# Performance work log

Hardware: AMD Instinct MI355X
Metric: run time of the kernel (lower is better)

## Reference

```python
import jax, jax.numpy as jnp
import numpy as np

EPS = 1e-5

def yat_dense(x, kernel, bias, alpha):
    # scaled by (sqrt(F)/log(1+F))**alpha, plus bias.
    y = x @ kernel  # [..., F]
    dist = jnp.sum(x * x, axis=-1, keepdims=True) + jnp.sum(kernel * kernel, axis=0) - 2.0 * y
    out = (y * y) / (dist + EPS)
    F = kernel.shape[1]
    scale = (jnp.sqrt(jnp.float32(F)) / jnp.log1p(jnp.float32(F))) ** alpha
    return out * scale + bias

def setup_inputs() -> dict:
    key = jax.random.key(0)
    ks = jax.random.split(key, 8)
    B, T, C = 8, 1024, 1024
    x = jax.random.normal(ks[0], (B, T, C), dtype=jnp.float32)
    mask = jnp.tril(jnp.ones((T, T), dtype=bool))[None, None, :, :]  # causal [1,1,T,T]
    W_attn = jax.random.normal(ks[1], (C, 3 * C), dtype=jnp.float32) * (C ** -0.5)
    b_attn = jnp.zeros((3 * C,), dtype=jnp.float32)
    alpha_attn = jnp.ones((1,), dtype=jnp.float32)
    W_proj = jax.random.normal(ks[2], (C, C), dtype=jnp.float32) * (C ** -0.5)
    b_proj = jnp.zeros((C,), dtype=jnp.float32)
    alpha_proj = jnp.ones((1,), dtype=jnp.float32)
    return {"x": x, "mask": mask, "W_attn": W_attn, "b_attn": b_attn,
            "alpha_attn": alpha_attn, "W_proj": W_proj, "b_proj": b_proj,
            "alpha_proj": alpha_proj}

def reference(x, mask, W_attn, b_attn, alpha_attn, W_proj, b_proj, alpha_proj):
    B, T, C = x.shape
    H = 16
    hd = C // H
    qkv = yat_dense(x, W_attn, b_attn, alpha_attn)           # [B,T,3C]
    qkv = qkv.reshape(B, T, 3 * H, hd)
    q, k, v = jnp.array_split(qkv, 3, axis=2)                # each [B,T,H,hd]
    scale = 1.0 / jnp.sqrt(jnp.float32(hd))
    attn = jnp.einsum('bqhd,bkhd->bhqk', q, k) * scale       # [B,H,T,T]
    attn = jnp.where(mask, attn, jnp.finfo(jnp.float32).min)
    attn = jax.nn.softmax(attn, axis=-1)
    out = jnp.einsum('bhqk,bkhd->bqhd', attn, v).reshape(B, T, C)
    out = yat_dense(out, W_proj, b_proj, alpha_proj)         # [B,T,C]
    return out
```

## Files before the change

### kernel.cpp

```cpp
#include <hip/hip_runtime.h>
#include <math.h>

#define EPS 1e-5f
#define QSCALE 0.18033688011f

typedef short s16x8 __attribute__((ext_vector_type(8)));
typedef float f32x4 __attribute__((ext_vector_type(4)));
typedef unsigned short ushort_t;
typedef unsigned int uint_t;

__device__ inline ushort_t f2bf(float f) {
  uint_t u = __float_as_uint(f);
  uint_t r = (u + 0x7fffu + ((u >> 16) & 1u)) >> 16;
  return (ushort_t)r;
}
__device__ inline float bf2f(ushort_t h) {
  return __uint_as_float(((uint_t)h) << 16);
}
__device__ inline uint_t cvtpk_bf16(float lo, float hi) {
  uint_t r;
  asm("v_cvt_pk_bf16_f32 %0, %1, %2" : "=v"(r) : "v"(lo), "v"(hi));
  return r;
}

__global__ __launch_bounds__(256) void cast_norm_k(const float* __restrict__ x,
                                                   ushort_t* __restrict__ xbf,
                                                   float* __restrict__ xnorm) {
  const int row = blockIdx.x * 4 + (threadIdx.x >> 6);
  const int lane = threadIdx.x & 63;
  const float4* p = (const float4*)(x + (size_t)row * 1024);
  ushort4* o = (ushort4*)(xbf + (size_t)row * 1024);
  float s = 0.f;
#pragma unroll
  for (int i = lane; i < 256; i += 64) {
    float4 v = p[i];
    s += v.x * v.x + v.y * v.y + v.z * v.z + v.w * v.w;
    o[i] = make_ushort4(f2bf(v.x), f2bf(v.y), f2bf(v.z), f2bf(v.w));
  }
#pragma unroll
  for (int off = 1; off < 64; off <<= 1) s += __shfl_xor(s, off, 64);
  if (lane == 0) xnorm[row] = s;
}

__global__ __launch_bounds__(256) void transpose_cast_k(
    const float* __restrict__ W, ushort_t* __restrict__ o, int K, int N) {
  __shared__ float t[32][33];
  const int n0 = blockIdx.x * 32, k0 = blockIdx.y * 32;
  const int tx = threadIdx.x & 31, ty = threadIdx.x >> 5;
#pragma unroll
  for (int j = 0; j < 4; ++j)
    t[ty + j * 8][tx] = W[(size_t)(k0 + ty + j * 8) * N + n0 + tx];
  __syncthreads();
#pragma unroll
  for (int j = 0; j < 4; ++j)
    o[(size_t)(n0 + ty + j * 8) * K + k0 + tx] = f2bf(t[tx][ty + j * 8]);
}

__global__ __launch_bounds__(256) void rownorm_bf16_k(const ushort_t* __restrict__ X,
                                                      float* __restrict__ out, int K) {
  const int row = blockIdx.x * 4 + (threadIdx.x >> 6);
  const int lane = threadIdx.x & 63;
  const ushort4* p = (const ushort4*)(X + (size_t)row * K);
  float s = 0.f;
  const int nq = K >> 2;
  for (int i = lane; i < nq; i += 64) {
    ushort4 v = p[i];
    float a = bf2f(v.x), b = bf2f(v.y), c = bf2f(v.z), d = bf2f(v.w);
    s += a * a + b * b + c * c + d * d;
  }
#pragma unroll
  for (int off = 1; off < 64; off <<= 1) s += __shfl_xor(s, off, 64);
  if (lane == 0) out[row] = s;
}

template <int MODE, int KK>
__global__ __launch_bounds__(256) void gemm_yat_mfma(
    const ushort_t* __restrict__ abf, const ushort_t* __restrict__ btbf,
    const float* __restrict__ bias, const float* __restrict__ alpha,
    const float* __restrict__ rown, const float* __restrict__ coln,
    void* __restrict__ outp, ushort_t* __restrict__ vtp, int M, int N) {
  __shared__ alignas(16) short lds[2 * 16384];

  const int tid = threadIdx.x;
  const int wid = tid >> 6;
  const int lane = tid & 63;
  const int g = lane >> 4;
  const int wm = wid >> 1, wn = wid & 1;

  const int nbx = gridDim.x;
  const int id = blockIdx.y * nbx + blockIdx.x;
  const int xcd = id & 7;
  const int sq = id >> 3;
  const int gq = sq >> 6;
  const int rr = sq & 63;
  const int bm = (xcd * 8 + (rr >> 3)) * 128;
  const int bn = (gq * 8 + (rr & 7)) * 128;

  f32x4 acc[4][4];
#pragma unroll
  for (int m = 0; m < 4; ++m)
#pragma unroll
    for (int n = 0; n < 4; ++n) acc[m][n] = (f32x4){0.f, 0.f, 0.f, 0.f};

  const int kc_sw = ((lane & 3) - ((lane >> 3) & 3)) & 3;
  const int slot_rd = (g + ((lane & 15) >> 1)) & 3;

  const ushort_t* srcb[8];
#pragma unroll
  for (int j = 0; j < 8; ++j) {
    const int q = wid + 4 * j;
    const int reg_idx = q >> 4;
    const int grp = (q >> 1) & 7;
    const int half = q & 1;
    const int grow = grp * 16 + (lane >> 2);
    const int gcol = half * 32 + kc_sw * 8;
    srcb[j] = (reg_idx == 0) ? abf + (size_t)(bm + grow) * KK + gcol
                             : btbf + (size_t)(bn + grow) * KK + gcol;
  }

  auto stage = [&](int buf, int t) {
#pragma unroll
    for (int j = 0; j < 8; ++j) {
      const int q = wid + 4 * j;
      const int reg_idx = q >> 4;
      const int grp = (q >> 1) & 7;
      const int half = q & 1;
      short* dst = &lds[buf * 16384 + reg_idx * 8192 + grp * 1024 + half * 512];
      __builtin_amdgcn_global_load_lds(
          (const __attribute__((address_space(1))) void*)(srcb[j] + t * 64),
          (__attribute__((address_space(3))) void*)dst, 16, 0, 0);
    }
  };

  stage(0, 0);
  stage(1, 1);

  constexpr int NT = KK / 64;
#pragma unroll
  for (int t = 0; t < NT; ++t) {
    const int cur = t & 1;
    if (t < NT - 1) {
      asm volatile("s_waitcnt vmcnt(8)" ::: "memory");
    } else {
      asm volatile("s_waitcnt vmcnt(0)" ::: "memory");
    }
    __builtin_amdgcn_sched_barrier(0);
    __builtin_amdgcn_s_barrier();

    s16x8 af[2][4], bfr[2][4];
#pragma unroll
    for (int kk = 0; kk < 2; ++kk) {
#pragma unroll
      for (int m = 0; m < 4; ++m) {
        const int off = cur * 16384 + (wm * 4 + m) * 1024 + kk * 512 +
                        (lane & 15) * 32 + slot_rd * 8;
        af[kk][m] = *(const s16x8*)&lds[off];
      }
#pragma unroll
      for (int n = 0; n < 4; ++n) {
        const int off = cur * 16384 + 8192 + (wn * 4 + n) * 1024 + kk * 512 +
                        (lane & 15) * 32 + slot_rd * 8;
        bfr[kk][n] = *(const s16x8*)&lds[off];
      }
    }
    __builtin_amdgcn_sched_barrier(0);
    asm volatile("s_waitcnt lgkmcnt(0)" ::: "memory");
    __builtin_amdgcn_sched_barrier(0);
    __builtin_amdgcn_s_barrier();

    if (t + 2 < NT) stage(cur, t + 2);

    __builtin_amdgcn_s_setprio(1);
#pragma unroll
    for (int kk = 0; kk < 2; ++kk)
#pragma unroll
      for (int m = 0; m < 4; ++m)
#pragma unroll
        for (int n = 0; n < 4; ++n)
          acc[m][n] = __builtin_amdgcn_mfma_f32_16x16x32_bf16(af[kk][m], bfr[kk][n],
                                                              acc[m][n], 0, 0, 0);
    __builtin_amdgcn_s_setprio(0);
  }

  const float sc = powf(sqrtf((float)N) / log1pf((float)N), alpha[0]);
  const int r0 = (lane >> 4) * 4;
  const int c0 = lane & 15;
#pragma unroll
  for (int m = 0; m < 4; ++m) {
    const int rowb = bm + wm * 64 + m * 16 + r0;
    float rn[4] = {rown[rowb], rown[rowb + 1], rown[rowb + 2], rown[rowb + 3]};
#pragma unroll
    for (int n = 0; n < 4; ++n) {
      const int col = bn + wn * 64 + n * 16 + c0;
      const float cn = coln[col];
      const float bs = bias[col];
      f32x4 a = acc[m][n];
      float o4[4];
#pragma unroll
      for (int r = 0; r < 4; ++r) {
        const float y = a[r];
        const float dist = rn[r] + cn - 2.f * y + EPS;
        o4[r] = (y * y) / dist * sc + bs;
      }
      if (MODE == 1) {
        if (col < 1024) {
#pragma unroll
          for (int r = 0; r < 4; ++r) o4[r] *= QSCALE;
        }
        if (col >= 2048) {
          const int d = col & 63, hh = (col >> 6) & 15;
          const int bb = rowb >> 10, t0 = rowb & 1023;
          ushort4 pk = make_ushort4(f2bf(o4[0]), f2bf(o4[1]), f2bf(o4[2]), f2bf(o4[3]));
          *(ushort4*)(vtp + (((size_t)(bb * 16 + hh) * 64 + d) << 10) + t0) = pk;
        } else {
#pragma unroll
          for (int r = 0; r < 4; ++r)
            ((ushort_t*)outp)[(size_t)(rowb + r) * N + col] = f2bf(o4[r]);
        }
      } else {
#pragma unroll
        for (int r = 0; r < 4; ++r)
          ((float*)outp)[(size_t)(rowb + r) * N + col] = o4[r];
      }
    }
  }
}

__global__ __launch_bounds__(256) void attn_mfma_k(const ushort_t* __restrict__ qkv,
                                                   const ushort_t* __restrict__ vt,
                                                   ushort_t* __restrict__ out) {
  const int i = blockIdx.y * 8 + blockIdx.x;
  const int xcd = i & 7, s = i >> 3;
  const int bh = xcd * 16 + (s & 15);
  const int pairx = s >> 4;
  const int b = bh >> 4, h = bh & 15;

  const int tid = threadIdx.x;
  const int wid = tid >> 6;
  const int lane = tid & 63;
  const int g = lane >> 4;
  const int c = lane & 15;

  __shared__ alignas(16) ushort_t Ks[64][76];
  __shared__ alignas(16) ushort_t Vs[64][76];
  __shared__ alignas(16) ushort_t Pl[4][16][76];

  const int srow = tid >> 3;
  const int sd0 = (tid & 7) * 8;
  const ushort_t* kbase = qkv + (size_t)(b * 1024) * 3072 + 1024 + h * 64;
  const ushort_t* vbase = vt + ((size_t)(b * 16 + h) << 16);

#pragma unroll
  for (int pass = 0; pass < 2; ++pass) {
    const int qt = pass == 0 ? pairx : 15 - pairx;

    const ushort_t* qrow =
        qkv + ((size_t)(b * 1024 + qt * 64 + wid * 16 + c)) * 3072 + h * 64;
    s16x8 qf[2];
    qf[0] = *(const s16x8*)(qrow + g * 8);
    qf[1] = *(const s16x8*)(qrow + 32 + g * 8);

    f32x4 acc_o[4];
#pragma unroll
    for (int dt = 0; dt < 4; ++dt) acc_o[dt] = (f32x4){0.f, 0.f, 0.f, 0.f};
    float l_lane = 0.f;

    s16x8 kreg[2], vreg[2];
#pragma unroll
    for (int ii = 0; ii < 2; ++ii) {
      kreg[ii] = *(const s16x8*)(kbase + (size_t)(srow + ii * 32) * 3072 + sd0);
      vreg[ii] = *(const s16x8*)(vbase + (size_t)(srow + ii * 32) * 1024 + sd0);
    }

    for (int kt = 0; kt <= qt; ++kt) {
      __syncthreads();
#pragma unroll
      for (int ii = 0; ii < 2; ++ii) {
        *(s16x8*)&Ks[srow + ii * 32][sd0] = kreg[ii];
        *(s16x8*)&Vs[srow + ii * 32][sd0] = vreg[ii];
      }
      __syncthreads();

      if (kt < qt) {
#pragma unroll
        for (int ii = 0; ii < 2; ++ii) {
          kreg[ii] = *(const s16x8*)(kbase +
                                     (size_t)((kt + 1) * 64 + srow + ii * 32) * 3072 + sd0);
          vreg[ii] = *(const s16x8*)(vbase + (size_t)(srow + ii * 32) * 1024 +
                                     (kt + 1) * 64 + sd0);
        }
      }

      const bool diag = (kt == qt);
      const int jtmax = diag ? wid : 3;

      f32x4 sacc[4];
#pragma unroll
      for (int jt = 0; jt < 4; ++jt) sacc[jt] = (f32x4){0.f, 0.f, 0.f, 0.f};
      __builtin_amdgcn_s_setprio(1);
#pragma unroll
      for (int jt = 0; jt < 4; ++jt) {
        if (jt <= jtmax) {
          s16x8 kf0 = *(const s16x8*)&Ks[jt * 16 + c][g * 8];
          s16x8 kf1 = *(const s16x8*)&Ks[jt * 16 + c][32 + g * 8];
          sacc[jt] = __builtin_amdgcn_mfma_f32_16x16x32_bf16(kf0, qf[0], sacc[jt], 0, 0, 0);
          sacc[jt] = __builtin_amdgcn_mfma_f32_16x16x32_bf16(kf1, qf[1], sacc[jt], 0, 0, 0);
        }
      }
      __builtin_amdgcn_s_setprio(0);

      float p[4][4];
      float rs = 0.f;
#pragma unroll
      for (int jt = 0; jt < 4; ++jt)
#pragma unroll
        for (int r = 0; r < 4; ++r) {
          float v = sacc[jt][r];
          if (diag && (jt * 16 + g * 4 + r > wid * 16 + c)) v = -INFINITY;
          const float e = exp2f(v);
          p[jt][r] = e;
          rs += e;
        }
      l_lane += rs;

#pragma unroll
      for (int jt = 0; jt < 4; ++jt) {
        uint2 w;
        w.x = cvtpk_bf16(p[jt][0], p[jt][1]);
        w.y = cvtpk_bf16(p[jt][2], p[jt][3]);
        *(uint2*)&Pl[wid][c][jt * 16 + g * 4] = w;
      }

      const int kcmax = diag ? (wid >> 1) : 1;
      __builtin_amdgcn_s_setprio(1);
#pragma unroll
      for (int kc = 0; kc < 2; ++kc) {
        if (kc <= kcmax) {
          s16x8 pf = *(const s16x8*)&Pl[wid][c][kc * 32 + g * 8];
#pragma unroll
          for (int dt = 0; dt < 4; ++dt) {
            s16x8 vf = *(const s16x8*)&Vs[dt * 16 + c][kc * 32 + g * 8];
            acc_o[dt] = __builtin_amdgcn_mfma_f32_16x16x32_bf16(pf, vf, acc_o[dt], 0, 0, 0);
          }
        }
      }
      __builtin_amdgcn_s_setprio(0);
    }

    float lt = l_lane;
    lt += __shfl_xor(lt, 16, 64);
    lt += __shfl_xor(lt, 32, 64);

    float l_bc[4];
#pragma unroll
    for (int r = 0; r < 4; ++r) l_bc[r] = __shfl(lt, g * 4 + r, 16);
#pragma unroll
    for (int r = 0; r < 4; ++r) {
      const float inv = 1.f / l_bc[r];
      ushort_t* op =
          out + ((size_t)(b * 1024 + qt * 64 + wid * 16 + g * 4 + r)) * 1024 + h * 64 + c;
#pragma unroll
      for (int dt = 0; dt < 4; ++dt) op[dt * 16] = f2bf(acc_o[dt][r] * inv);
    }
  }
}

extern "C" void kernel_launch(void* const* d_in, const int* in_sizes, int n_in,
                              void* d_out, int out_size, void* d_ws, size_t ws_size,
                              hipStream_t stream) {
  const float* x = (const float*)d_in[0];
  const float* W_attn = (const float*)d_in[2];
  const float* b_attn = (const float*)d_in[3];
  const float* alpha_attn = (const float*)d_in[4];
  const float* W_proj = (const float*)d_in[5];
  const float* b_proj = (const float*)d_in[6];
  const float* alpha_proj = (const float*)d_in[7];
  float* out = (float*)d_out;

  char* ws = (char*)d_ws;
  ushort_t* qkv = (ushort_t*)(ws);
  ushort_t* attnout = (ushort_t*)(ws + 50331648ull);
  ushort_t* xbf = (ushort_t*)(ws + 67108864ull);
  ushort_t* watt = (ushort_t*)(ws + 83886080ull);
  ushort_t* wpjt = (ushort_t*)(ws + 90177536ull);
  float* xnorm = (float*)(ws + 92274688ull);
  float* anorm = (float*)(ws + 92307456ull);
  float* watn = (float*)(ws + 92340224ull);
  float* wpn = (float*)(ws + 92352512ull);
  ushort_t* vt = (ushort_t*)(ws + 92372992ull);

  const int M = 8192;

  cast_norm_k<<<M / 4, 256, 0, stream>>>(x, xbf, xnorm);
  transpose_cast_k<<<dim3(96, 32), 256, 0, stream>>>(W_attn, watt, 1024, 3072);
  transpose_cast_k<<<dim3(32, 32), 256, 0, stream>>>(W_proj, wpjt, 1024, 1024);
  rownorm_bf16_k<<<3072 / 4, 256, 0, stream>>>(watt, watn, 1024);
  rownorm_bf16_k<<<1024 / 4, 256, 0, stream>>>(wpjt, wpn, 1024);

  gemm_yat_mfma<1, 1024><<<dim3(3072 / 128, M / 128), 256, 0, stream>>>(
      xbf, watt, b_attn, alpha_attn, xnorm, watn, (void*)qkv, vt, M, 3072);

  attn_mfma_k<<<dim3(8, 128), 256, 0, stream>>>(qkv, vt, attnout);

  rownorm_bf16_k<<<M / 4, 256, 0, stream>>>(attnout, anorm, 1024);

  gemm_yat_mfma<0, 1024><<<dim3(1024 / 128, M / 128), 256, 0, stream>>>(
      attnout, wpjt, b_proj, alpha_proj, anorm, wpn, (void*)out, nullptr, M, 1024);
}
```

Measured before the change: 158.1 us.

## Use triple-buffered 32-wide K tiles with a single barrier per step

The GEMM main loop moves from a double-buffered 64-wide K tile to a triple-buffered 32-wide K tile. The ring of three buffers lets the prefetch of tile t+2 be issued right after one barrier, dropping the second barrier and the explicit lgkmcnt wait that previously kept the buffer from being overwritten. This cuts synchronisation per step and LDS use per block, which may help occupancy. In exchange there are twice as many loop iterations and fewer MFMAs per barrier, so fixed per-iteration overhead rises.

```diff
diff --git a/kernel.cpp b/kernel.cpp
--- a/kernel.cpp
+++ b/kernel.cpp
@@ -79,7 +79,7 @@
     const float* __restrict__ bias, const float* __restrict__ alpha,
     const float* __restrict__ rown, const float* __restrict__ coln,
     void* __restrict__ outp, ushort_t* __restrict__ vtp, int M, int N) {
-  __shared__ alignas(16) short lds[2 * 16384];
+  __shared__ alignas(16) short lds[3 * 8192];
 
   const int tid = threadIdx.x;
   const int wid = tid >> 6;
@@ -105,29 +105,27 @@
   const int kc_sw = ((lane & 3) - ((lane >> 3) & 3)) & 3;
   const int slot_rd = (g + ((lane & 15) >> 1)) & 3;
 
-  const ushort_t* srcb[8];
-#pragma unroll
-  for (int j = 0; j < 8; ++j) {
+  const ushort_t* srcb[4];
+#pragma unroll
+  for (int j = 0; j < 4; ++j) {
     const int q = wid + 4 * j;
-    const int reg_idx = q >> 4;
-    const int grp = (q >> 1) & 7;
-    const int half = q & 1;
-    const int grow = grp * 16 + (lane >> 2);
-    const int gcol = half * 32 + kc_sw * 8;
+    const int reg_idx = q >> 3;
+    const int i = q & 7;
+    const int grow = i * 16 + (lane >> 2);
+    const int gcol = kc_sw * 8;
     srcb[j] = (reg_idx == 0) ? abf + (size_t)(bm + grow) * KK + gcol
                              : btbf + (size_t)(bn + grow) * KK + gcol;
   }
 
   auto stage = [&](int buf, int t) {
 #pragma unroll
-    for (int j = 0; j < 8; ++j) {
+    for (int j = 0; j < 4; ++j) {
       const int q = wid + 4 * j;
-      const int reg_idx = q >> 4;
-      const int grp = (q >> 1) & 7;
-      const int half = q & 1;
-      short* dst = &lds[buf * 16384 + reg_idx * 8192 + grp * 1024 + half * 512];
+      const int reg_idx = q >> 3;
+      const int i = q & 7;
+      short* dst = &lds[buf * 8192 + reg_idx * 4096 + i * 512];
       __builtin_amdgcn_global_load_lds(
-          (const __attribute__((address_space(1))) void*)(srcb[j] + t * 64),
+          (const __attribute__((address_space(1))) void*)(srcb[j] + t * 32),
           (__attribute__((address_space(3))) void*)dst, 16, 0, 0);
     }
   };
@@ -135,50 +133,37 @@
   stage(0, 0);
   stage(1, 1);
 
-  constexpr int NT = KK / 64;
+  constexpr int NT = KK / 32;
 #pragma unroll
   for (int t = 0; t < NT; ++t) {
-    const int cur = t & 1;
+    const int cur = t % 3;
     if (t < NT - 1) {
-      asm volatile("s_waitcnt vmcnt(8)" ::: "memory");
+      asm volatile("s_waitcnt vmcnt(4)" ::: "memory");
     } else {
       asm volatile("s_waitcnt vmcnt(0)" ::: "memory");
     }
+    __builtin_amdgcn_s_barrier();
     __builtin_amdgcn_sched_barrier(0);
-    __builtin_amdgcn_s_barrier();
-
-    s16x8 af[2][4], bfr[2][4];
-#pragma unroll
-    for (int kk = 0; kk < 2; ++kk) {
-#pragma unroll
-      for (int m = 0; m < 4; ++m) {
-        const int off = cur * 16384 + (wm * 4 + m) * 1024 + kk * 512 +
-                        (lane & 15) * 32 + slot_rd * 8;
-        af[kk][m] = *(const s16x8*)&lds[off];
-      }
-#pragma unroll
-      for (int n = 0; n < 4; ++n) {
-        const int off = cur * 16384 + 8192 + (wn * 4 + n) * 1024 + kk * 512 +
-                        (lane & 15) * 32 + slot_rd * 8;
-        bfr[kk][n] = *(const s16x8*)&lds[off];
-      }
-    }
-    __builtin_amdgcn_sched_barrier(0);
-    asm volatile("s_waitcnt lgkmcnt(0)" ::: "memory");
-    __builtin_amdgcn_sched_barrier(0);
-    __builtin_amdgcn_s_barrier();
-
-    if (t + 2 < NT) stage(cur, t + 2);
-
+    if (t + 2 < NT) stage((t + 2) % 3, t + 2);
+
+    s16x8 af[4], bfr[4];
+#pragma unroll
+    for (int m = 0; m < 4; ++m) {
+      const int off = cur * 8192 + (wm * 4 + m) * 512 + (lane & 15) * 32 + slot_rd * 8;
+      af[m] = *(const s16x8*)&lds[off];
+    }
+#pragma unroll
+    for (int n = 0; n < 4; ++n) {
+      const int off = cur * 8192 + 4096 + (wn * 4 + n) * 512 + (lane & 15) * 32 + slot_rd * 8;
+      bfr[n] = *(const s16x8*)&lds[off];
+    }
     __builtin_amdgcn_s_setprio(1);
 #pragma unroll
-    for (int kk = 0; kk < 2; ++kk)
-#pragma unroll
-      for (int m = 0; m < 4; ++m)
-#pragma unroll
-        for (int n = 0; n < 4; ++n)
-          acc[m][n] = __builtin_amdgcn_mfma_f32_16x16x32_bf16(af[kk][m], bfr[kk][n],
-                                                              acc[m][n], 0, 0, 0);
+    for (int m = 0; m < 4; ++m)
+#pragma unroll
+      for (int n = 0; n < 4; ++n)
+        acc[m][n] = __builtin_amdgcn_mfma_f32_16x16x32_bf16(af[m], bfr[n],
+                                                            acc[m][n], 0, 0, 0);
     __builtin_amdgcn_s_setprio(0);
   }
 
```

Result: slower. 161.8 us (+2.4%).
